# Performance work log

Hardware: AMD Instinct MI355X
Metric: run time of the kernel (lower is better)

Reference implementation:

```python
import jax, jax.numpy as jnp
import numpy as np

B = 64        # graphs
N0 = 2048     # nodes per graph
DEG = 16      # avg degree
IN = 128      # input_dim
H = 30        # hcs
NH = 11       # heads
OD = 8        # output_dim[i]
K1, K2, K3 = 1844, 1660, 1494  # ceil(0.9*n) chain


def setup_inputs() -> dict:
    key = jax.random.key(0)
    ks = jax.random.split(key, 32)
    N = B * N0
    E = N * DEG
    x = jax.random.normal(ks[0], (N, IN), jnp.float32)
    g = jnp.repeat(jnp.arange(B, dtype=jnp.int32), N0 * DEG)
    src = g * N0 + jax.random.randint(ks[1], (E,), 0, N0, dtype=jnp.int32)
    dst = g * N0 + jax.random.randint(ks[2], (E,), 0, N0, dtype=jnp.int32)
    edge_index = jnp.stack([src, dst])
    edge_attr = jax.random.uniform(ks[3], (E,), jnp.float32)
    batch = jnp.repeat(jnp.arange(B, dtype=jnp.int32), N0)
    s = 0.05
    def W(k, *shape):
        return jax.random.normal(k, shape, jnp.float32) * s
    return {
        'x': x, 'edge_index': edge_index, 'edge_attr': edge_attr, 'batch': batch,
        'ln_g': jnp.ones((IN,), jnp.float32), 'ln_b': jnp.zeros((IN,), jnp.float32),
        'W_rel1': W(ks[4], IN, H), 'b_rel1': W(ks[5], H), 'W_root1': W(ks[6], IN, H),
        'W_rel2': W(ks[7], H, H), 'b_rel2': W(ks[8], H), 'W_root2': W(ks[9], H, H),
        'W_rel3': W(ks[10], H, H), 'b_rel3': W(ks[11], H), 'W_root3': W(ks[12], H, H),
        'pool_w1': W(ks[13], H), 'pool_w2': W(ks[14], H), 'pool_w3': W(ks[15], H),
        'head_W1': W(ks[16], NH, 2 * H, 8 * H), 'head_b1': W(ks[17], NH, 8 * H),
        'head_W2': W(ks[18], NH, 8 * H, 32 * H), 'head_b2': W(ks[19], NH, 32 * H),
        'head_W3': W(ks[20], NH, 32 * H, OD), 'head_b3': W(ks[21], NH, OD),
    }


def _layernorm(x, g, b):
    m = x.mean(-1, keepdims=True)
    v = ((x - m) ** 2).mean(-1, keepdims=True)
    return (x - m) * jax.lax.rsqrt(v + 1e-5) * g + b


def _gconv(x, src, dst, ew, Wr, br, Ws, N):
    # PyG GraphConv: out = lin_rel(sum_j ew*x_j) + lin_root(x)
    agg = jax.ops.segment_sum(x[src] * ew[:, None], dst, num_segments=N)
    return agg @ Wr + br + x @ Ws


def _topk_pool(x, src, dst, ew, w, n, k):
    # score = tanh(x.w/||w||); keep top-k per graph; gate kept nodes by score
    score = jnp.tanh((x @ w) / jnp.linalg.norm(w)).reshape(B, n)
    vals, idx = jax.lax.top_k(score, k)                      # [B,k]
    xg = x.reshape(B, n, -1)
    xk = jnp.take_along_axis(xg, idx[:, :, None], axis=1) * vals[:, :, None]
    x_new = xk.reshape(B * k, -1)
    newidx = jnp.full((B, n), -1, jnp.int32)
    newidx = newidx.at[jnp.arange(B)[:, None], idx].set(
        jnp.broadcast_to(jnp.arange(k, dtype=jnp.int32), (B, k)))
    g = src // n
    ns = newidx[g, src % n]
    nd = newidx[g, dst % n]
    keep = (ns >= 0) & (nd >= 0)
    src_new = jnp.where(keep, g * k + ns, 0)
    dst_new = jnp.where(keep, g * k + nd, 0)
    ew_new = jnp.where(keep, ew, 0.0)
    return x_new, src_new, dst_new, ew_new


def _readout(x, k):
    xg = x.reshape(B, k, -1)
    return jnp.concatenate([xg.max(axis=1), xg.mean(axis=1)], axis=1)  # [B,2H]


def reference(x, edge_index, edge_attr, batch, ln_g, ln_b,
              W_rel1, b_rel1, W_root1, W_rel2, b_rel2, W_root2,
              W_rel3, b_rel3, W_root3, pool_w1, pool_w2, pool_w3,
              head_W1, head_b1, head_W2, head_b2, head_W3, head_b3):
    src, dst = edge_index[0], edge_index[1]
    ew = edge_attr
    h = _layernorm(x, ln_g, ln_b)

    h = jax.nn.relu(_gconv(h, src, dst, ew, W_rel1, b_rel1, W_root1, B * N0))
    h, src, dst, ew = _topk_pool(h, src, dst, ew, pool_w1, N0, K1)
    x1 = _readout(h, K1)

    h = jax.nn.relu(_gconv(h, src, dst, ew, W_rel2, b_rel2, W_root2, B * K1))
    h, src, dst, ew = _topk_pool(h, src, dst, ew, pool_w2, K1, K2)
    x2 = _readout(h, K2)

    h = jax.nn.relu(_gconv(h, src, dst, ew, W_rel3, b_rel3, W_root3, B * K2))
    h, src, dst, ew = _topk_pool(h, src, dst, ew, pool_w3, K2, K3)
    x3 = _readout(h, K3)

    z = jax.nn.relu(x1 + x2 + x3)                                   # [B,60]
    a = jax.nn.relu(jnp.einsum('bd,hdo->hbo', z, head_W1) + head_b1[:, None, :])
    a = jax.nn.relu(jnp.einsum('hbo,hop->hbp', a, head_W2) + head_b2[:, None, :])
    out = jnp.einsum('hbp,hpq->hbq', a, head_W3) + head_b3[:, None, :]
    return out  # [11, B, 8]
```

## Files before the change

### kernel.cpp

```cpp
#include <hip/hip_runtime.h>
#include <hip/hip_bf16.h>

#define B 64
#define N0 2048
#define DEG 16
#define IN_DIM 128
#define H 30
#define NH 11
#define K1 1844
#define K2 1660
#define K3 1494
#define NTOT (B * N0)
#define ETOT (NTOT * DEG)
#define EPG (ETOT / B)
#define RSTRIDE 32
#define ESTRIDE1 32768
#define RSEG 16

__global__ __launch_bounds__(256) void k_prep(
    const float* __restrict__ ln_g, const float* __restrict__ ln_b,
    const float* __restrict__ Wrel1, const float* __restrict__ brel1, const float* __restrict__ Wroot1,
    const float* __restrict__ Wrel2, const float* __restrict__ Wroot2,
    const float* __restrict__ Wrel3, const float* __restrict__ Wroot3,
    float* __restrict__ Wc1, float* __restrict__ S1, float* __restrict__ T1,
    float* __restrict__ Wc2, float* __restrict__ Wc3)
{
    int tid = threadIdx.x;
    for (int i = tid; i < IN_DIM * 60; i += 256) {
        int j = i / 60, c = i - j * 60;
        float w = (c < H) ? Wrel1[j * H + c] : Wroot1[j * H + (c - H)];
        Wc1[i] = w * ln_g[j];
    }
    if (tid < 60) {
        int c = tid;
        float s = 0.f, tt = 0.f;
        for (int j = 0; j < IN_DIM; ++j) {
            float w = (c < H) ? Wrel1[j * H + c] : Wroot1[j * H + (c - H)];
            s += w * ln_g[j];
            tt += w * ln_b[j];
        }
        S1[c] = s;
        T1[c] = (c < H) ? tt : tt + brel1[c - H];
    }
    for (int i = tid; i < H * 60; i += 256) {
        int j = i / 60, c = i - j * 60;
        Wc2[i] = (c < H) ? Wrel2[j * H + c] : Wroot2[j * H + (c - H)];
        Wc3[i] = (c < H) ? Wrel3[j * H + c] : Wroot3[j * H + (c - H)];
    }
}

__global__ __launch_bounds__(256) void k_lnproj(
    const float* __restrict__ x, const float* __restrict__ Wc,
    const float* __restrict__ S, const float* __restrict__ T,
    float* __restrict__ r, float* __restrict__ t)
{
    __shared__ float wlds[4][IN_DIM][16];
    for (int i = threadIdx.x; i < IN_DIM * 64; i += 256) {
        int k = i >> 6, cc = i & 63;
        int cg = cc >> 4, j = cc & 15;
        wlds[cg][k][j] = (j < 15) ? Wc[k * 60 + cg * 15 + j] : 0.f;
    }
    __syncthreads();
    int lane = threadIdx.x & 63, cg = threadIdx.x >> 6;
    int row0 = blockIdx.x * 512 + lane;
    const float* xb = x + (size_t)row0 * IN_DIM;
    float acc[8][15];
    float sum[8], sumsq[8];
#pragma unroll
    for (int ri = 0; ri < 8; ++ri) {
        sum[ri] = 0.f; sumsq[ri] = 0.f;
#pragma unroll
        for (int c = 0; c < 15; ++c) acc[ri][c] = 0.f;
    }
    float4 cur[8], nxt[8];
#pragma unroll
    for (int ri = 0; ri < 8; ++ri)
        cur[ri] = *(const float4*)(xb + (size_t)ri * 64 * IN_DIM);
    for (int kb = 0; kb < 32; ++kb) {
        if (kb < 31) {
#pragma unroll
            for (int ri = 0; ri < 8; ++ri)
                nxt[ri] = *(const float4*)(xb + (size_t)ri * 64 * IN_DIM + (kb + 1) * 4);
        }
#pragma unroll
        for (int kk = 0; kk < 4; ++kk) {
            int k = kb * 4 + kk;
            float4 w0 = *(const float4*)&wlds[cg][k][0];
            float4 w1 = *(const float4*)&wlds[cg][k][4];
            float4 w2 = *(const float4*)&wlds[cg][k][8];
            float4 w3 = *(const float4*)&wlds[cg][k][12];
#pragma unroll
            for (int ri = 0; ri < 8; ++ri) {
                float xv = (kk == 0) ? cur[ri].x : (kk == 1) ? cur[ri].y
                          : (kk == 2) ? cur[ri].z : cur[ri].w;
                sum[ri] += xv; sumsq[ri] += xv * xv;
                acc[ri][0]  += xv * w0.x; acc[ri][1]  += xv * w0.y;
                acc[ri][2]  += xv * w0.z; acc[ri][3]  += xv * w0.w;
                acc[ri][4]  += xv * w1.x; acc[ri][5]  += xv * w1.y;
                acc[ri][6]  += xv * w1.z; acc[ri][7]  += xv * w1.w;
                acc[ri][8]  += xv * w2.x; acc[ri][9]  += xv * w2.y;
                acc[ri][10] += xv * w2.z; acc[ri][11] += xv * w2.w;
                acc[ri][12] += xv * w3.x; acc[ri][13] += xv * w3.y;
                acc[ri][14] += xv * w3.z;
            }
        }
        if (kb < 31) {
#pragma unroll
            for (int ri = 0; ri < 8; ++ri) cur[ri] = nxt[ri];
        }
    }
    bool isR = (cg < 2);
    int cbase = (cg & 1) * 15;
    float* outp = isR ? r : t;
    float sS[15], sT[15];
#pragma unroll
    for (int c = 0; c < 15; ++c) { sS[c] = S[cg * 15 + c]; sT[c] = T[cg * 15 + c]; }
#pragma unroll
    for (int ri = 0; ri < 8; ++ri) {
        int row = row0 + ri * 64;
        float mean = sum[ri] * (1.f / 128.f);
        float var = sumsq[ri] * (1.f / 128.f) - mean * mean;
        float rstd = 1.0f / sqrtf(var + 1e-5f);
        float* op = outp + (size_t)row * RSTRIDE + cbase;
#pragma unroll
        for (int c = 0; c < 15; ++c)
            op[c] = rstd * (acc[ri][c] - mean * sS[c]) + sT[c];
        if (cg & 1) {
            outp[(size_t)row * RSTRIDE + 30] = 0.f;
            outp[(size_t)row * RSTRIDE + 31] = 0.f;
        }
    }
}

__global__ __launch_bounds__(256) void k_proj30p(
    const float* __restrict__ hbuf, const int* __restrict__ sidx,
    const float* __restrict__ score, const float* __restrict__ Wc,
    const float* __restrict__ brel, float* __restrict__ r, float* __restrict__ t,
    int n_old, int k)
{
    __shared__ float wlds[4][32][16];
    for (int i = threadIdx.x; i < 30 * 64; i += 256) {
        int m = i >> 6, cc = i & 63;
        int cg = cc >> 4, j = cc & 15;
        wlds[cg][m][j] = (j < 15) ? Wc[m * 60 + cg * 15 + j] : 0.f;
    }
    __syncthreads();
    int lane = threadIdx.x & 63, cg = threadIdx.x >> 6;
    int row0 = blockIdx.x * 256 + lane;
    float acc[4][15];
#pragma unroll
    for (int ri = 0; ri < 4; ++ri)
#pragma unroll
        for (int c = 0; c < 15; ++c) acc[ri][c] = 0.f;
    float vals[4];
    const float* hp[4];
#pragma unroll
    for (int ri = 0; ri < 4; ++ri) {
        int row = row0 + ri * 64;
        int g = row / k, j = row - g * k;
        int idx = sidx[g * k + j];
        vals[ri] = score[g * n_old + idx];
        hp[ri] = hbuf + (size_t)(g * n_old + idx) * RSTRIDE;
    }
    for (int mb = 0; mb < 7; ++mb) {
        float4 cur[4];
#pragma unroll
        for (int ri = 0; ri < 4; ++ri) cur[ri] = *(const float4*)(hp[ri] + mb * 4);
#pragma unroll
        for (int kk = 0; kk < 4; ++kk) {
            int m = mb * 4 + kk;
            float4 w0 = *(const float4*)&wlds[cg][m][0];
            float4 w1 = *(const float4*)&wlds[cg][m][4];
            float4 w2 = *(const float4*)&wlds[cg][m][8];
            float4 w3 = *(const float4*)&wlds[cg][m][12];
#pragma unroll
            for (int ri = 0; ri < 4; ++ri) {
                float xv = (kk == 0) ? cur[ri].x : (kk == 1) ? cur[ri].y
                          : (kk == 2) ? cur[ri].z : cur[ri].w;
                acc[ri][0]  += xv * w0.x; acc[ri][1]  += xv * w0.y;
                acc[ri][2]  += xv * w0.z; acc[ri][3]  += xv * w0.w;
                acc[ri][4]  += xv * w1.x; acc[ri][5]  += xv * w1.y;
                acc[ri][6]  += xv * w1.z; acc[ri][7]  += xv * w1.w;
                acc[ri][8]  += xv * w2.x; acc[ri][9]  += xv * w2.y;
                acc[ri][10] += xv * w2.z; acc[ri][11] += xv * w2.w;
                acc[ri][12] += xv * w3.x; acc[ri][13] += xv * w3.y;
                acc[ri][14] += xv * w3.z;
            }
        }
    }
    {
        float2 h2[4];
#pragma unroll
        for (int ri = 0; ri < 4; ++ri) h2[ri] = *(const float2*)(hp[ri] + 28);
#pragma unroll
        for (int kk = 0; kk < 2; ++kk) {
            int m = 28 + kk;
            float4 w0 = *(const float4*)&wlds[cg][m][0];
            float4 w1 = *(const float4*)&wlds[cg][m][4];
            float4 w2 = *(const float4*)&wlds[cg][m][8];
            float4 w3 = *(const float4*)&wlds[cg][m][12];
#pragma unroll
            for (int ri = 0; ri < 4; ++ri) {
                float xv = (kk == 0) ? h2[ri].x : h2[ri].y;
                acc[ri][0]  += xv * w0.x; acc[ri][1]  += xv * w0.y;
                acc[ri][2]  += xv * w0.z; acc[ri][3]  += xv * w0.w;
                acc[ri][4]  += xv * w1.x; acc[ri][5]  += xv * w1.y;
                acc[ri][6]  += xv * w1.z; acc[ri][7]  += xv * w1.w;
                acc[ri][8]  += xv * w2.x; acc[ri][9]  += xv * w2.y;
                acc[ri][10] += xv * w2.z; acc[ri][11] += xv * w2.w;
                acc[ri][12] += xv * w3.x; acc[ri][13] += xv * w3.y;
                acc[ri][14] += xv * w3.z;
            }
        }
    }
    bool isR = (cg < 2);
    int cbase = (cg & 1) * 15;
    float* outp = isR ? r : t;
    float sB[15];
#pragma unroll
    for (int c = 0; c < 15; ++c) sB[c] = isR ? 0.f : brel[cbase + c];
#pragma unroll
    for (int ri = 0; ri < 4; ++ri) {
        int row = row0 + ri * 64;
        float val = vals[ri];
        float* op = outp + (size_t)row * RSTRIDE + cbase;
#pragma unroll
        for (int c = 0; c < 15; ++c)
            op[c] = val * acc[ri][c] + sB[c];
        if (cg & 1) {
            outp[(size_t)row * RSTRIDE + 30] = 0.f;
            outp[(size_t)row * RSTRIDE + 31] = 0.f;
        }
    }
}

__global__ __launch_bounds__(1024) void k_hist1(
    const int* __restrict__ dst, unsigned short* __restrict__ rank,
    int* __restrict__ chunkCnt)
{
    __shared__ unsigned int cnt[2048];
    int chunk = blockIdx.x, g = chunk >> 2;
    for (int i = threadIdx.x; i < 2048; i += 1024) cnt[i] = 0;
    __syncthreads();
    int e0 = chunk * 8192;
#pragma unroll
    for (int u = 0; u < 8; ++u) {
        int e = e0 + u * 1024 + threadIdx.x;
        int d = dst[e] - g * N0;
        rank[e] = (unsigned short)atomicAdd(&cnt[d], 1u);
    }
    __syncthreads();
    for (int i = threadIdx.x; i < 2048; i += 1024) chunkCnt[chunk * 2048 + i] = cnt[i];
}

__global__ __launch_bounds__(1024) void k_scan(
    int* __restrict__ chunkCnt, int* __restrict__ runStart, int* __restrict__ runLen)
{
    __shared__ int bufA[2048], bufB[2048];
    int g = blockIdx.x;
    int c0[2], c1[2], c2[2], tt[2];
    for (int h2 = 0; h2 < 2; ++h2) {
        int d = threadIdx.x + h2 * 1024;
        c0[h2] = chunkCnt[(g * 4 + 0) * 2048 + d];
        c1[h2] = chunkCnt[(g * 4 + 1) * 2048 + d];
        c2[h2] = chunkCnt[(g * 4 + 2) * 2048 + d];
        int c3 = chunkCnt[(g * 4 + 3) * 2048 + d];
        tt[h2] = c0[h2] + c1[h2] + c2[h2] + c3;
        bufA[d] = tt[h2];
    }
    __syncthreads();
    int* s_ = bufA; int* d_ = bufB;
    for (int off = 1; off < 2048; off <<= 1) {
        for (int h2 = 0; h2 < 2; ++h2) {
            int d = threadIdx.x + h2 * 1024;
            int v = s_[d];
            if (d >= off) v += s_[d - off];
            d_[d] = v;
        }
        __syncthreads();
        int* tmp = s_; s_ = d_; d_ = tmp;
    }
    for (int h2 = 0; h2 < 2; ++h2) {
        int d = threadIdx.x + h2 * 1024;
        int ex = s_[d] - tt[h2];
        runStart[g * 2048 + d] = ex;
        runLen[g * 2048 + d] = tt[h2];
        chunkCnt[(g * 4 + 0) * 2048 + d] = ex;
        chunkCnt[(g * 4 + 1) * 2048 + d] = ex + c0[h2];
        chunkCnt[(g * 4 + 2) * 2048 + d] = ex + c0[h2] + c1[h2];
        chunkCnt[(g * 4 + 3) * 2048 + d] = ex + c0[h2] + c1[h2] + c2[h2];
    }
}

__global__ __launch_bounds__(1024) void k_scat1(
    const int* __restrict__ src, const int* __restrict__ dst, const float* __restrict__ ew,
    const unsigned short* __restrict__ rank, const int* __restrict__ chunkOff,
    float2* __restrict__ sOut)
{
    int chunk = blockIdx.x, g = chunk >> 2;
    int e0 = chunk * 8192;
#pragma unroll
    for (int u = 0; u < 8; ++u) {
        int e = e0 + u * 1024 + threadIdx.x;
        int d = dst[e] - g * N0;
        int pos = chunkOff[chunk * 2048 + d] + (int)rank[e];
        sOut[(size_t)g * ESTRIDE1 + pos] = make_float2(__int_as_float(src[e]), ew[e]);
    }
}

template<int LVL>
__global__ __launch_bounds__(256) void k_gather(
    const float2* __restrict__ sE, const int* __restrict__ runS, const int* __restrict__ runL,
    const int* __restrict__ ind1, const int* __restrict__ ind2, const int* __restrict__ mapc,
    const float* __restrict__ rp, const float* __restrict__ t, float* __restrict__ h,
    const float* __restrict__ poolw, float* __restrict__ score,
    int n, int rK, int nblocks)
{
    int b = blockIdx.x;
    int cpx = nblocks >> 3;
    b = (b & 7) * cpx + (b >> 3);
    int slot = threadIdx.x >> 5, j = threadIdx.x & 31;
    int v = b * 8 + slot;
    int g = v / n;
    int local = v - g * n;
    int v1 = local;
    if (LVL >= 2) v1 = ind2[g * K2 + v1];
    if (LVL >= 1) v1 = ind1[g * K1 + v1];
    int s0 = runS[g * 2048 + v1], len = runL[g * 2048 + v1];
    const float2* meta = sE + (size_t)g * ESTRIDE1 + s0;
    int rbase = g * rK;
    float acc = 0.f;
    for (int c = 0; c < len; c += 8) {
        int lim = len - c; if (lim > 8) lim = 8;
        float2 m[8];
#pragma unroll
        for (int u = 0; u < 8; ++u) m[u] = meta[c + (u < lim ? u : 0)];
        int rowv[8]; float wv[8];
#pragma unroll
        for (int u = 0; u < 8; ++u) {
            int srcg = __float_as_int(m[u].x);
            float w = (u < lim) ? m[u].y : 0.f;
            if (LVL == 0) {
                rowv[u] = srcg;
            } else {
                int ss = mapc[srcg];
                rowv[u] = rbase + (ss < 0 ? 0 : ss);
                w = (ss < 0) ? 0.f : w;
            }
            wv[u] = w;
        }
#pragma unroll
        for (int u = 0; u < 8; ++u)
            acc += rp[(size_t)rowv[u] * RSTRIDE + j] * wv[u];
    }
    float wj = (j < H) ? poolw[j] : 0.f;
    float hval = 0.f;
    if (j < H) {
        hval = fmaxf(acc + t[(size_t)v * RSTRIDE + j], 0.f);
        h[(size_t)v * RSTRIDE + j] = hval;
    }
    float p = hval * wj, q = wj * wj;
#pragma unroll
    for (int off = 16; off > 0; off >>= 1) {
        p += __shfl_xor(p, off, 32);
        q += __shfl_xor(q, off, 32);
    }
    if (j == 0) score[v] = tanhf(p / sqrtf(q));
}

__global__ __launch_bounds__(1024) void k_topk_map(
    const float* __restrict__ score, int* __restrict__ sidx, int* __restrict__ mapc,
    int n, int k, int first)
{
    __shared__ unsigned long long keys[2048];
    __shared__ int inv[2048];
    int g = blockIdx.x;
    for (int i = threadIdx.x; i < 2048; i += 1024) {
        unsigned long long key = ~0ull;
        if (i < n) {
            float s = score[g * n + i];
            if (s == 0.f) s = 0.f;
            unsigned u = __float_as_uint(s);
            unsigned asc = (u & 0x80000000u) ? ~u : (u | 0x80000000u);
            unsigned desc = ~asc;
            key = ((unsigned long long)desc << 32) | (unsigned)i;
        }
        keys[i] = key;
        inv[i] = -1;
    }
    __syncthreads();
    for (int kk = 2; kk <= 2048; kk <<= 1) {
        for (int jj = kk >> 1; jj > 0; jj >>= 1) {
            for (int i = threadIdx.x; i < 2048; i += 1024) {
                int ixj = i ^ jj;
                if (ixj > i) {
                    unsigned long long a = keys[i], bb = keys[ixj];
                    bool up = ((i & kk) == 0);
                    if ((a > bb) == up) { keys[i] = bb; keys[ixj] = a; }
                }
            }
            __syncthreads();
        }
    }
    for (int j = threadIdx.x; j < k; j += 1024) {
        int idx = (int)(keys[j] & 0xffffffffu);
        sidx[g * k + j] = idx;
        inv[idx] = j;
    }
    __syncthreads();
    if (first) {
        for (int v = threadIdx.x; v < N0; v += 1024)
            mapc[g * N0 + v] = inv[v];
    } else {
        for (int v = threadIdx.x; v < N0; v += 1024) {
            int m = mapc[g * N0 + v];
            mapc[g * N0 + v] = (m >= 0) ? inv[m] : -1;
        }
    }
}

__global__ __launch_bounds__(256) void k_rpart(
    const float* __restrict__ hbuf, const int* __restrict__ sidx,
    const float* __restrict__ score, float* __restrict__ pmax, float* __restrict__ psum,
    int n_old, int k)
{
    __shared__ float smax[8][32], ssum[8][32];
    int g = blockIdx.y, seg = blockIdx.x;
    int clen = (k + RSEG - 1) / RSEG;
    int start = seg * clen;
    int end = start + clen; if (end > k) end = k;
    int f = threadIdx.x & 31, rr = threadIdx.x >> 5;
    float mx = -INFINITY, sm = 0.f;
    if (f < H) {
        for (int j = start + rr; j < end; j += 8) {
            int idx = sidx[g * k + j];
            float val = score[g * n_old + idx];
            float v = hbuf[(size_t)(g * n_old + idx) * RSTRIDE + f] * val;
            mx = fmaxf(mx, v);
            sm += v;
        }
    }
    smax[rr][f] = mx; ssum[rr][f] = sm;
    __syncthreads();
    if (rr == 0) {
        for (int q = 1; q < 8; ++q) { mx = fmaxf(mx, smax[q][f]); sm += ssum[q][f]; }
        pmax[(g * RSEG + seg) * 32 + f] = mx;
        psum[(g * RSEG + seg) * 32 + f] = sm;
    }
}

__global__ __launch_bounds__(64) void k_zfin(
    const float* __restrict__ pm1, const float* __restrict__ ps1,
    const float* __restrict__ pm2, const float* __restrict__ ps2,
    const float* __restrict__ pm3, const float* __restrict__ ps3,
    float* __restrict__ z)
{
    int g = blockIdx.x, c = threadIdx.x;
    if (c >= 60) return;
    float v1, v2, v3;
    if (c < H) {
        float m1 = -INFINITY, m2 = -INFINITY, m3 = -INFINITY;
        for (int s = 0; s < RSEG; ++s) {
            m1 = fmaxf(m1, pm1[(g * RSEG + s) * 32 + c]);
            m2 = fmaxf(m2, pm2[(g * RSEG + s) * 32 + c]);
            m3 = fmaxf(m3, pm3[(g * RSEG + s) * 32 + c]);
        }
        v1 = m1; v2 = m2; v3 = m3;
    } else {
        int f = c - H;
        float s1 = 0.f, s2 = 0.f, s3 = 0.f;
        for (int s = 0; s < RSEG; ++s) {
            s1 += ps1[(g * RSEG + s) * 32 + f];
            s2 += ps2[(g * RSEG + s) * 32 + f];
            s3 += ps3[(g * RSEG + s) * 32 + f];
        }
        v1 = s1 / (float)K1; v2 = s2 / (float)K2; v3 = s3 / (float)K3;
    }
    z[g * 60 + c] = fmaxf(v1 + v2 + v3, 0.f);
}

__global__ __launch_bounds__(256) void k_mlp1(
    const float* __restrict__ z, const float* __restrict__ W,
    const float* __restrict__ bias, float* __restrict__ a)
{
    int hb = blockIdx.x, hh = hb >> 6, b = hb & 63;
    __shared__ float zr[60];
    if (threadIdx.x < 60) zr[threadIdx.x] = z[b * 60 + threadIdx.x];
    __syncthreads();
    int o = threadIdx.x;
    if (o < 240) {
        float acc = bias[hh * 240 + o];
        const float* Wp = W + hh * 60 * 240;
#pragma unroll
        for (int d = 0; d < 60; ++d) acc += zr[d] * Wp[d * 240 + o];
        a[(hh * B + b) * 240 + o] = fmaxf(acc, 0.f);
    }
}

__global__ __launch_bounds__(256) void k_mlp2(
    const float* __restrict__ a1, const float* __restrict__ W,
    const float* __restrict__ bias, float* __restrict__ a2)
{
    __shared__ float a1t[64 * 240];
    int hh = blockIdx.x / 15, ct = blockIdx.x % 15;
    const float4* ag = (const float4*)(a1 + (size_t)hh * B * 240);
    for (int i = threadIdx.x; i < 64 * 240 / 4; i += 256)
        ((float4*)a1t)[i] = ag[i];
    __syncthreads();
    int col = threadIdx.x & 63, rg = threadIdx.x >> 6;
    const float* Wp = W + (size_t)hh * 240 * 960 + ct * 64 + col;
    float acc[16];
#pragma unroll
    for (int i = 0; i < 16; ++i) acc[i] = 0.f;
#pragma unroll 4
    for (int o = 0; o < 240; ++o) {
        float w = Wp[(size_t)o * 960];
        const float* ar = &a1t[0];
#pragma unroll
        for (int i = 0; i < 16; ++i)
            acc[i] += w * ar[(rg * 16 + i) * 240 + o];
    }
    float bv = bias[hh * 960 + ct * 64 + col];
#pragma unroll
    for (int i = 0; i < 16; ++i)
        a2[((size_t)hh * B + rg * 16 + i) * 960 + ct * 64 + col] =
            fmaxf(acc[i] + bv, 0.f);
}

__global__ __launch_bounds__(64) void k_mlp3(
    const float* __restrict__ a2, const float* __restrict__ W,
    const float* __restrict__ bias, float* __restrict__ out)
{
    int hb = blockIdx.x, hh = hb >> 6, b = hb & 63;
    __shared__ float ar[960];
    __shared__ float part[64];
    for (int i = threadIdx.x; i < 960; i += 64) ar[i] = a2[(hh * B + b) * 960 + i];
    __syncthreads();
    int q = threadIdx.x & 7, c = threadIdx.x >> 3;
    const float* Wp = W + hh * 960 * 8;
    float acc = 0.f;
    for (int p = c; p < 960; p += 8) acc += ar[p] * Wp[p * 8 + q];
    part[threadIdx.x] = acc;
    __syncthreads();
    if (threadIdx.x < 8) {
        float s = bias[hh * 8 + threadIdx.x];
        for (int cc = 0; cc < 8; ++cc) s += part[cc * 8 + threadIdx.x];
        out[(hh * B + b) * 8 + threadIdx.x] = s;
    }
}

extern "C" void kernel_launch(void* const* d_in, const int* in_sizes, int n_in,
                              void* d_out, int out_size, void* d_ws, size_t ws_size,
                              hipStream_t stream)
{
    const float* x       = (const float*)d_in[0];
    const int*   eidx    = (const int*)d_in[1];
    const int*   src0    = eidx;
    const int*   dst0    = eidx + ETOT;
    const float* ew0     = (const float*)d_in[2];
    const float* ln_g    = (const float*)d_in[4];
    const float* ln_b    = (const float*)d_in[5];
    const float* W_rel1  = (const float*)d_in[6];
    const float* b_rel1  = (const float*)d_in[7];
    const float* W_root1 = (const float*)d_in[8];
    const float* W_rel2  = (const float*)d_in[9];
    const float* b_rel2  = (const float*)d_in[10];
    const float* W_root2 = (const float*)d_in[11];
    const float* W_rel3  = (const float*)d_in[12];
    const float* b_rel3  = (const float*)d_in[13];
    const float* W_root3 = (const float*)d_in[14];
    const float* pool_w1 = (const float*)d_in[15];
    const float* pool_w2 = (const float*)d_in[16];
    const float* pool_w3 = (const float*)d_in[17];
    const float* head_W1 = (const float*)d_in[18];
    const float* head_b1 = (const float*)d_in[19];
    const float* head_W2 = (const float*)d_in[20];
    const float* head_b2 = (const float*)d_in[21];
    const float* head_W3 = (const float*)d_in[22];
    const float* head_b3 = (const float*)d_in[23];

    float* ws     = (float*)d_ws;
    float* rbuf   = ws;
    float* tbuf   = rbuf + (size_t)NTOT * RSTRIDE;
    float* abuf   = tbuf + (size_t)NTOT * RSTRIDE;
    float2* sA    = (float2*)(abuf + (size_t)NTOT * RSTRIDE);
    float* score  = (float*)(sA + (size_t)B * ESTRIDE1);
    int*   sidxA  = (int*)(score + NTOT);
    int*   sidxB  = sidxA + B * K1;
    int*   sidxC  = sidxB + B * K2;
    int*   mapc   = sidxC + B * K3;
    int*   runSA  = mapc + NTOT;
    int*   runLA  = runSA + B * 2048;
    float* pm1    = (float*)(runLA + B * 2048);
    float* ps1    = pm1 + B * RSEG * 32;
    float* pm2    = ps1 + B * RSEG * 32;
    float* ps2    = pm2 + B * RSEG * 32;
    float* pm3    = ps2 + B * RSEG * 32;
    float* ps3    = pm3 + B * RSEG * 32;
    float* zb     = ps3 + B * RSEG * 32;
    float* Wc1    = zb + B * 60;
    float* S1     = Wc1 + IN_DIM * 60;
    float* T1     = S1 + 60;
    float* Wc2    = T1 + 60;
    float* Wc3    = Wc2 + H * 60;
    int* chunkBuf         = (int*)abuf;
    unsigned short* rank  = (unsigned short*)((char*)abuf + (4u << 20));
    float* a1 = rbuf;
    float* a2 = a1 + NH * B * 240;

    k_prep<<<1, 256, 0, stream>>>(ln_g, ln_b, W_rel1, b_rel1, W_root1,
                                  W_rel2, W_root2, W_rel3, W_root3,
                                  Wc1, S1, T1, Wc2, Wc3);

    k_hist1<<<256, 1024, 0, stream>>>(dst0, rank, chunkBuf);
    k_scan<<<B, 1024, 0, stream>>>(chunkBuf, runSA, runLA);
    k_scat1<<<256, 1024, 0, stream>>>(src0, dst0, ew0, rank, chunkBuf, sA);

    k_lnproj<<<NTOT / 512, 256, 0, stream>>>(x, Wc1, S1, T1, rbuf, tbuf);
    k_gather<0><<<NTOT / 8, 256, 0, stream>>>(sA, runSA, runLA, nullptr, nullptr, nullptr,
                                              rbuf, tbuf, abuf, pool_w1, score,
                                              N0, N0, NTOT / 8);
    k_topk_map<<<B, 1024, 0, stream>>>(score, sidxA, mapc, N0, K1, 1);
    k_rpart<<<dim3(RSEG, B), 256, 0, stream>>>(abuf, sidxA, score, pm1, ps1, N0, K1);
    k_proj30p<<<B * K1 / 256, 256, 0, stream>>>(abuf, sidxA, score, Wc2, b_rel2,
                                                rbuf, tbuf, N0, K1);

    k_gather<1><<<B * K1 / 8, 256, 0, stream>>>(sA, runSA, runLA, sidxA, nullptr, mapc,
                                                rbuf, tbuf, abuf, pool_w2, score,
                                                K1, K1, B * K1 / 8);
    k_topk_map<<<B, 1024, 0, stream>>>(score, sidxB, mapc, K1, K2, 0);
    k_rpart<<<dim3(RSEG, B), 256, 0, stream>>>(abuf, sidxB, score, pm2, ps2, K1, K2);
    k_proj30p<<<B * K2 / 256, 256, 0, stream>>>(abuf, sidxB, score, Wc3, b_rel3,
                                                rbuf, tbuf, K1, K2);

    k_gather<2><<<B * K2 / 8, 256, 0, stream>>>(sA, runSA, runLA, sidxA, sidxB, mapc,
                                                rbuf, tbuf, abuf, pool_w3, score,
                                                K2, K2, B * K2 / 8);
    k_topk_map<<<B, 1024, 0, stream>>>(score, sidxC, mapc, K2, K3, 0);
    k_rpart<<<dim3(RSEG, B), 256, 0, stream>>>(abuf, sidxC, score, pm3, ps3, K2, K3);

    k_zfin<<<B, 64, 0, stream>>>(pm1, ps1, pm2, ps2, pm3, ps3, zb);
    k_mlp1<<<NH * B, 256, 0, stream>>>(zb, head_W1, head_b1, a1);
    k_mlp2<<<NH * 15, 256, 0, stream>>>(a1, head_W2, head_b2, a2);
    k_mlp3<<<NH * B, 64, 0, stream>>>(a2, head_W3, head_b3, (float*)d_out);
}
```

Baseline: 570.5 us.

## Interleave rel/root projections into one buffer and rewrite LN projection per-wave

Merges the separate r and t projection buffers into one interleaved row of 64 floats (rel at 0..29, root at 32..61), so the gather reads neighbor rel values and its own root value from the same row. The LayerNorm+projection kernel is rewritten so each lane owns one output column, keeps its 128 weights in registers, and walks 64 rows per wave, using wave shuffles for mean and variance and broadcast float4 row loads. This trades the old register-blocked 8-row tile for simpler per-row work with coalesced 60-wide stores, at the cost of high register pressure and redundant row loads per lane. The zero-padding stores are dropped.

```diff
diff --git a/kernel.cpp b/kernel.cpp
--- a/kernel.cpp
+++ b/kernel.cpp
@@ -12,8 +12,8 @@
 #define K3 1494
 #define NTOT (B * N0)
 #define ETOT (NTOT * DEG)
-#define EPG (ETOT / B)
 #define RSTRIDE 32
+#define RT 64
 #define ESTRIDE1 32768
 #define RSEG 16
 
@@ -52,90 +52,60 @@
 __global__ __launch_bounds__(256) void k_lnproj(
     const float* __restrict__ x, const float* __restrict__ Wc,
     const float* __restrict__ S, const float* __restrict__ T,
-    float* __restrict__ r, float* __restrict__ t)
-{
-    __shared__ float wlds[4][IN_DIM][16];
-    for (int i = threadIdx.x; i < IN_DIM * 64; i += 256) {
-        int k = i >> 6, cc = i & 63;
-        int cg = cc >> 4, j = cc & 15;
-        wlds[cg][k][j] = (j < 15) ? Wc[k * 60 + cg * 15 + j] : 0.f;
-    }
-    __syncthreads();
-    int lane = threadIdx.x & 63, cg = threadIdx.x >> 6;
-    int row0 = blockIdx.x * 512 + lane;
-    const float* xb = x + (size_t)row0 * IN_DIM;
-    float acc[8][15];
-    float sum[8], sumsq[8];
-#pragma unroll
-    for (int ri = 0; ri < 8; ++ri) {
-        sum[ri] = 0.f; sumsq[ri] = 0.f;
-#pragma unroll
-        for (int c = 0; c < 15; ++c) acc[ri][c] = 0.f;
-    }
-    float4 cur[8], nxt[8];
-#pragma unroll
-    for (int ri = 0; ri < 8; ++ri)
-        cur[ri] = *(const float4*)(xb + (size_t)ri * 64 * IN_DIM);
-    for (int kb = 0; kb < 32; ++kb) {
-        if (kb < 31) {
-#pragma unroll
-            for (int ri = 0; ri < 8; ++ri)
-                nxt[ri] = *(const float4*)(xb + (size_t)ri * 64 * IN_DIM + (kb + 1) * 4);
-        }
-#pragma unroll
-        for (int kk = 0; kk < 4; ++kk) {
-            int k = kb * 4 + kk;
-            float4 w0 = *(const float4*)&wlds[cg][k][0];
-            float4 w1 = *(const float4*)&wlds[cg][k][4];
-            float4 w2 = *(const float4*)&wlds[cg][k][8];
-            float4 w3 = *(const float4*)&wlds[cg][k][12];
-#pragma unroll
-            for (int ri = 0; ri < 8; ++ri) {
-                float xv = (kk == 0) ? cur[ri].x : (kk == 1) ? cur[ri].y
-                          : (kk == 2) ? cur[ri].z : cur[ri].w;
-                sum[ri] += xv; sumsq[ri] += xv * xv;
-                acc[ri][0]  += xv * w0.x; acc[ri][1]  += xv * w0.y;
-                acc[ri][2]  += xv * w0.z; acc[ri][3]  += xv * w0.w;
-                acc[ri][4]  += xv * w1.x; acc[ri][5]  += xv * w1.y;
-                acc[ri][6]  += xv * w1.z; acc[ri][7]  += xv * w1.w;
-                acc[ri][8]  += xv * w2.x; acc[ri][9]  += xv * w2.y;
-                acc[ri][10] += xv * w2.z; acc[ri][11] += xv * w2.w;
-                acc[ri][12] += xv * w3.x; acc[ri][13] += xv * w3.y;
-                acc[ri][14] += xv * w3.z;
-            }
-        }
-        if (kb < 31) {
-#pragma unroll
-            for (int ri = 0; ri < 8; ++ri) cur[ri] = nxt[ri];
-        }
-    }
-    bool isR = (cg < 2);
-    int cbase = (cg & 1) * 15;
-    float* outp = isR ? r : t;
-    float sS[15], sT[15];
-#pragma unroll
-    for (int c = 0; c < 15; ++c) { sS[c] = S[cg * 15 + c]; sT[c] = T[cg * 15 + c]; }
-#pragma unroll
-    for (int ri = 0; ri < 8; ++ri) {
-        int row = row0 + ri * 64;
-        float mean = sum[ri] * (1.f / 128.f);
-        float var = sumsq[ri] * (1.f / 128.f) - mean * mean;
+    float* __restrict__ rt)
+{
+    __shared__ float wlds[IN_DIM * 60];
+    for (int i = threadIdx.x; i < IN_DIM * 60 / 4; i += 256)
+        ((float4*)wlds)[i] = ((const float4*)Wc)[i];
+    __syncthreads();
+    int lane = threadIdx.x & 63;
+    int wid = __builtin_amdgcn_readfirstlane(threadIdx.x >> 6);
+    int c = (lane < 60) ? lane : 59;
+    float wreg[IN_DIM];
+#pragma unroll
+    for (int k = 0; k < IN_DIM; ++k) wreg[k] = wlds[k * 60 + c];
+    float Sc = S[c], Tc = T[c];
+    int outc = (c < 30) ? c : c + 2;
+    int rowbase = (blockIdx.x * 4 + wid) * 64;
+    for (int rr = 0; rr < 64; ++rr) {
+        int row = rowbase + rr;
+        const float4* xr4 = (const float4*)(x + (size_t)row * IN_DIM);
+        float xa = x[(size_t)row * IN_DIM + lane];
+        float xb = x[(size_t)row * IN_DIM + 64 + lane];
+        float s1 = xa + xb;
+        float s2 = xa * xa + xb * xb;
+#pragma unroll
+        for (int off = 32; off > 0; off >>= 1) {
+            s1 += __shfl_xor(s1, off, 64);
+            s2 += __shfl_xor(s2, off, 64);
+        }
+        float mean = s1 * (1.f / 128.f);
+        float var = s2 * (1.f / 128.f) - mean * mean;
         float rstd = 1.0f / sqrtf(var + 1e-5f);
-        float* op = outp + (size_t)row * RSTRIDE + cbase;
-#pragma unroll
-        for (int c = 0; c < 15; ++c)
-            op[c] = rstd * (acc[ri][c] - mean * sS[c]) + sT[c];
-        if (cg & 1) {
-            outp[(size_t)row * RSTRIDE + 30] = 0.f;
-            outp[(size_t)row * RSTRIDE + 31] = 0.f;
-        }
+        float acc0 = 0.f, acc1 = 0.f;
+#pragma unroll
+        for (int q = 0; q < 32; q += 2) {
+            float4 xq0 = xr4[q];
+            float4 xq1 = xr4[q + 1];
+            acc0 = fmaf(xq0.x, wreg[q * 4 + 0], acc0);
+            acc1 = fmaf(xq1.x, wreg[q * 4 + 4], acc1);
+            acc0 = fmaf(xq0.y, wreg[q * 4 + 1], acc0);
+            acc1 = fmaf(xq1.y, wreg[q * 4 + 5], acc1);
+            acc0 = fmaf(xq0.z, wreg[q * 4 + 2], acc0);
+            acc1 = fmaf(xq1.z, wreg[q * 4 + 6], acc1);
+            acc0 = fmaf(xq0.w, wreg[q * 4 + 3], acc0);
+            acc1 = fmaf(xq1.w, wreg[q * 4 + 7], acc1);
+        }
+        float outv = rstd * ((acc0 + acc1) - mean * Sc) + Tc;
+        if (lane < 60)
+            rt[(size_t)row * RT + outc] = outv;
     }
 }
 
 __global__ __launch_bounds__(256) void k_proj30p(
     const float* __restrict__ hbuf, const int* __restrict__ sidx,
     const float* __restrict__ score, const float* __restrict__ Wc,
-    const float* __restrict__ brel, float* __restrict__ r, float* __restrict__ t,
+    const float* __restrict__ brel, float* __restrict__ rt,
     int n_old, int k)
 {
     __shared__ float wlds[4][32][16];
@@ -214,23 +184,18 @@
         }
     }
     bool isR = (cg < 2);
-    int cbase = (cg & 1) * 15;
-    float* outp = isR ? r : t;
+    int coff = (isR ? 0 : 32) + (cg & 1) * 15;
     float sB[15];
 #pragma unroll
-    for (int c = 0; c < 15; ++c) sB[c] = isR ? 0.f : brel[cbase + c];
+    for (int c = 0; c < 15; ++c) sB[c] = isR ? 0.f : brel[(cg & 1) * 15 + c];
 #pragma unroll
     for (int ri = 0; ri < 4; ++ri) {
         int row = row0 + ri * 64;
         float val = vals[ri];
-        float* op = outp + (size_t)row * RSTRIDE + cbase;
+        float* op = rt + (size_t)row * RT + coff;
 #pragma unroll
         for (int c = 0; c < 15; ++c)
             op[c] = val * acc[ri][c] + sB[c];
-        if (cg & 1) {
-            outp[(size_t)row * RSTRIDE + 30] = 0.f;
-            outp[(size_t)row * RSTRIDE + 31] = 0.f;
-        }
     }
 }
 
@@ -312,7 +277,7 @@
 __global__ __launch_bounds__(256) void k_gather(
     const float2* __restrict__ sE, const int* __restrict__ runS, const int* __restrict__ runL,
     const int* __restrict__ ind1, const int* __restrict__ ind2, const int* __restrict__ mapc,
-    const float* __restrict__ rp, const float* __restrict__ t, float* __restrict__ h,
+    const float* __restrict__ rt, float* __restrict__ h,
     const float* __restrict__ poolw, float* __restrict__ score,
     int n, int rK, int nblocks)
 {
@@ -351,12 +316,12 @@
         }
 #pragma unroll
         for (int u = 0; u < 8; ++u)
-            acc += rp[(size_t)rowv[u] * RSTRIDE + j] * wv[u];
+            acc += rt[(size_t)rowv[u] * RT + j] * wv[u];
     }
     float wj = (j < H) ? poolw[j] : 0.f;
     float hval = 0.f;
     if (j < H) {
-        hval = fmaxf(acc + t[(size_t)v * RSTRIDE + j], 0.f);
+        hval = fmaxf(acc + rt[(size_t)v * RT + 32 + j], 0.f);
         h[(size_t)v * RSTRIDE + j] = hval;
     }
     float p = hval * wj, q = wj * wj;
@@ -580,9 +545,8 @@
     const float* head_b3 = (const float*)d_in[23];
 
     float* ws     = (float*)d_ws;
-    float* rbuf   = ws;
-    float* tbuf   = rbuf + (size_t)NTOT * RSTRIDE;
-    float* abuf   = tbuf + (size_t)NTOT * RSTRIDE;
+    float* rtbuf  = ws;
+    float* abuf   = rtbuf + (size_t)NTOT * RT;
     float2* sA    = (float2*)(abuf + (size_t)NTOT * RSTRIDE);
     float* score  = (float*)(sA + (size_t)B * ESTRIDE1);
     int*   sidxA  = (int*)(score + NTOT);
@@ -605,7 +569,7 @@
     float* Wc3    = Wc2 + H * 60;
     int* chunkBuf         = (int*)abuf;
     unsigned short* rank  = (unsigned short*)((char*)abuf + (4u << 20));
-    float* a1 = rbuf;
+    float* a1 = rtbuf;
     float* a2 = a1 + NH * B * 240;
 
     k_prep<<<1, 256, 0, stream>>>(ln_g, ln_b, W_rel1, b_rel1, W_root1,
@@ -616,25 +580,25 @@
     k_scan<<<B, 1024, 0, stream>>>(chunkBuf, runSA, runLA);
     k_scat1<<<256, 1024, 0, stream>>>(src0, dst0, ew0, rank, chunkBuf, sA);
 
-    k_lnproj<<<NTOT / 512, 256, 0, stream>>>(x, Wc1, S1, T1, rbuf, tbuf);
+    k_lnproj<<<NTOT / 256, 256, 0, stream>>>(x, Wc1, S1, T1, rtbuf);
     k_gather<0><<<NTOT / 8, 256, 0, stream>>>(sA, runSA, runLA, nullptr, nullptr, nullptr,
-                                              rbuf, tbuf, abuf, pool_w1, score,
+                                              rtbuf, abuf, pool_w1, score,
                                               N0, N0, NTOT / 8);
     k_topk_map<<<B, 1024, 0, stream>>>(score, sidxA, mapc, N0, K1, 1);
     k_rpart<<<dim3(RSEG, B), 256, 0, stream>>>(abuf, sidxA, score, pm1, ps1, N0, K1);
     k_proj30p<<<B * K1 / 256, 256, 0, stream>>>(abuf, sidxA, score, Wc2, b_rel2,
-                                                rbuf, tbuf, N0, K1);
+                                                rtbuf, N0, K1);
 
     k_gather<1><<<B * K1 / 8, 256, 0, stream>>>(sA, runSA, runLA, sidxA, nullptr, mapc,
-                                                rbuf, tbuf, abuf, pool_w2, score,
+                                                rtbuf, abuf, pool_w2, score,
                                                 K1, K1, B * K1 / 8);
     k_topk_map<<<B, 1024, 0, stream>>>(score, sidxB, mapc, K1, K2, 0);
     k_rpart<<<dim3(RSEG, B), 256, 0, stream>>>(abuf, sidxB, score, pm2, ps2, K1, K2);
     k_proj30p<<<B * K2 / 256, 256, 0, stream>>>(abuf, sidxB, score, Wc3, b_rel3,
-                                                rbuf, tbuf, K1, K2);
+                                                rtbuf, K1, K2);
 
     k_gather<2><<<B * K2 / 8, 256, 0, stream>>>(sA, runSA, runLA, sidxA, sidxB, mapc,
-                                                rbuf, tbuf, abuf, pool_w3, score,
+                                                rtbuf, abuf, pool_w3, score,
                                                 K2, K2, B * K2 / 8);
     k_topk_map<<<B, 1024, 0, stream>>>(score, sidxC, mapc, K2, K3, 0);
     k_rpart<<<dim3(RSEG, B), 256, 0, stream>>>(abuf, sidxC, score, pm3, ps3, K2, K3);
```

Result: no change. 568.0 us (-0.4%).
